# Optimization experiments

Measured on AMD Instinct MI355X. Metric: run time of the kernel, lower is better.

## Reference

```python
import jax, jax.numpy as jnp
from jax import lax
import numpy as np

N, K, F, H, NG, T = 32768, 16, 64, 128, 1024, 2


def setup_inputs() -> dict:
    key = jax.random.key(0)
    ks = jax.random.split(key, 24)
    def rn(k, shape, s=0.05):
        return jax.random.normal(k, shape, jnp.float32) * s
    inp = {
        'n': jax.random.normal(ks[0], (N, F), jnp.float32),
        'nbr': jax.random.randint(ks[1], (N, K), 0, N),
        # deterministic sorted graph ids -> every graph non-empty (safe segment_max)
        'gid': (jnp.arange(N) * NG) // N,
        'G': NG,
        # SAGEConv layer 1: LSTM(F,F), fc_self/fc_neigh F->H
        'lstm1_Wih': rn(ks[2], (F, 4 * F)), 'lstm1_Whh': rn(ks[3], (F, 4 * F)), 'lstm1_b': jnp.zeros((4 * F,), jnp.float32),
        'fcs1_W': rn(ks[4], (F, H)), 'fcs1_b': jnp.zeros((H,), jnp.float32),
        'fcn1_W': rn(ks[5], (F, H)), 'fcn1_b': jnp.zeros((H,), jnp.float32),
        # SAGEConv layer 2: LSTM(H,H), fc_self/fc_neigh H->H
        'lstm2_Wih': rn(ks[6], (H, 4 * H)), 'lstm2_Whh': rn(ks[7], (H, 4 * H)), 'lstm2_b': jnp.zeros((4 * H,), jnp.float32),
        'fcs2_W': rn(ks[8], (H, H)), 'fcs2_b': jnp.zeros((H,), jnp.float32),
        'fcn2_W': rn(ks[9], (H, H)), 'fcn2_b': jnp.zeros((H,), jnp.float32),
        # WeightedSumAndMax atom weighting: H->1
        'rw_W': rn(ks[10], (H, 1)), 'rw_b': jnp.zeros((1,), jnp.float32),
        # task head: 2H->H, H->T
        'h1_W': rn(ks[11], (2 * H, H)), 'h1_b': jnp.zeros((H,), jnp.float32),
        'h2_W': rn(ks[12], (H, T)), 'h2_b': jnp.zeros((T,), jnp.float32),
    }
    return inp


def _lstm_last(xseq, Wih, Whh, b):
    # xseq: [N, K, Fin]; returns last hidden state [N, Hh]
    Hh = Whh.shape[0]
    h0 = jnp.zeros((xseq.shape[0], Hh), xseq.dtype)
    def step(carry, xt):
        h, c = carry
        g = xt @ Wih + h @ Whh + b  # [N, 4H], torch gate order i,f,g,o
        i, f, gg, o = jnp.split(g, 4, axis=-1)
        c = jax.nn.sigmoid(f) * c + jax.nn.sigmoid(i) * jnp.tanh(gg)
        h = jax.nn.sigmoid(o) * jnp.tanh(c)
        return (h, c), None
    (h, _), _ = lax.scan(step, (h0, h0), jnp.swapaxes(xseq, 0, 1))
    return h


def _sage_layer(x, nbr, Wih, Whh, b, Ws, bs, Wn, bn):
    hn = _lstm_last(x[nbr], Wih, Whh, b)          # LSTM aggregate of neighbors
    return jax.nn.sigmoid(x @ Ws + bs + hn @ Wn + bn)


def reference(n, nbr, gid, G,
              lstm1_Wih, lstm1_Whh, lstm1_b, fcs1_W, fcs1_b, fcn1_W, fcn1_b,
              lstm2_Wih, lstm2_Whh, lstm2_b, fcs2_W, fcs2_b, fcn2_W, fcn2_b,
              rw_W, rw_b, h1_W, h1_b, h2_W, h2_b):
    G = int(G)
    h1 = _sage_layer(n, nbr, lstm1_Wih, lstm1_Whh, lstm1_b, fcs1_W, fcs1_b, fcn1_W, fcn1_b)
    h2 = _sage_layer(h1, nbr, lstm2_Wih, lstm2_Whh, lstm2_b, fcs2_W, fcs2_b, fcn2_W, fcn2_b)
    # WeightedSumAndMax readout
    w = jax.nn.sigmoid(h2 @ rw_W + rw_b)                       # [N,1]
    wsum = jax.ops.segment_sum(w * h2, gid, num_segments=G)    # [G,H]
    mx = jax.ops.segment_max(h2, gid, num_segments=G)          # [G,H]
    gemb = jnp.concatenate([wsum, mx], axis=-1)                # [G,2H]
    y = jax.nn.sigmoid(gemb @ h1_W + h1_b)
    y = jax.nn.sigmoid(y @ h2_W + h2_b)                        # classification
    return y
```

## Files before the change

### kernel.cpp

```cpp
#include <hip/hip_runtime.h>

typedef unsigned short u16;
typedef __attribute__((ext_vector_type(8))) short bf16x8;
typedef __attribute__((ext_vector_type(4))) float f32x4;
typedef __attribute__((ext_vector_type(2))) float f32x2;

constexpr int N_ = 32768;
constexpr int H_ = 128;
constexpr int G_ = 1024;
constexpr int T_ = 2;

__device__ __forceinline__ float sigf(float x){
  float e = __builtin_amdgcn_exp2f(x * -1.44269504f);
  return __builtin_amdgcn_rcpf(1.0f + e);
}
__device__ __forceinline__ f32x2 sig2(f32x2 x){
  f32x2 t = x * -1.44269504f;
  f32x2 e; e.x = __builtin_amdgcn_exp2f(t.x); e.y = __builtin_amdgcn_exp2f(t.y);
  f32x2 d = e + 1.0f;
  f32x2 r; r.x = __builtin_amdgcn_rcpf(d.x); r.y = __builtin_amdgcn_rcpf(d.y);
  return r;
}
__device__ __forceinline__ f32x2 tanh2(f32x2 x){
  f32x2 t = x * 2.88539008f;
  f32x2 e; e.x = __builtin_amdgcn_exp2f(t.x); e.y = __builtin_amdgcn_exp2f(t.y);
  f32x2 d = e + 1.0f;
  f32x2 r; r.x = __builtin_amdgcn_rcpf(d.x); r.y = __builtin_amdgcn_rcpf(d.y);
  return 1.0f - 2.0f*r;
}
__device__ __forceinline__ u16 f2bf(float f){
  unsigned u = __float_as_uint(f);
  unsigned r = (u + 0x7FFFu + ((u>>16)&1u))>>16;
  return (u16)r;
}
__device__ __forceinline__ unsigned cvt_pk_bf16(float a, float b){
  unsigned r;
  asm("v_cvt_pk_bf16_f32 %0, %1, %2" : "=v"(r) : "v"(a), "v"(b));
  return r;
}
__device__ __forceinline__ float bf2f(u16 h){ return __uint_as_float(((unsigned)h)<<16); }
__device__ __forceinline__ float asf(unsigned u){ return __uint_as_float(u); }
__device__ __forceinline__ f32x4 mfma16(bf16x8 a, bf16x8 b, f32x4 c){
  return __builtin_amdgcn_mfma_f32_16x16x32_bf16(a,b,c,0,0,0);
}

__global__ __launch_bounds__(64)
void pack_all(const float* __restrict__ l1Wih, const float* __restrict__ fcs1W,
              const float* __restrict__ l1Whh, const float* __restrict__ fcn1W,
              const float* __restrict__ l2Wih, const float* __restrict__ fcs2W,
              const float* __restrict__ l2Whh, const float* __restrict__ fcn2W,
              const float* __restrict__ l1b, const float* __restrict__ bs1,
              const float* __restrict__ bn1,
              const float* __restrict__ l2b, const float* __restrict__ bs2,
              const float* __restrict__ bn2,
              u16* BY1, u16* BW1, u16* BN1, u16* BY2, u16* BW2, u16* BN2,
              u16* bY1, u16* bY2)
{
  int b = blockIdx.x;
  const int lane = threadIdx.x;
  if (b == 416) {
    for (int i = lane; i < 1024; i += 64) {
      if (i < 384) {
        int p = i; float v;
        if (p < 256) { int o = (p&3)*64 + ((p>>6)<<4) + ((p>>2)&15); v = l1b[o]; }
        else         { int j = p-256; v = bs1[j] + bn1[j]; }
        bY1[p] = f2bf(v);
      } else {
        int p = i - 384; float v;
        if (p < 512) { int o = (p&3)*128 + ((p>>6)<<4) + ((p>>2)&15); v = l2b[o]; }
        else         { int j = p-512; v = bs2[j] + bn2[j]; }
        bY2[p] = f2bf(v);
      }
    }
    return;
  }
  const float* src; u16* dst; int srcNC, NTtot, ntOff, ntCnt, Fh, perm;
  if      (b < 32)  { src=l1Wih; dst=BY1; srcNC=256; NTtot=24; ntOff=0;  ntCnt=16; Fh=64;  perm=2; }
  else if (b < 48)  { src=fcs1W; dst=BY1; srcNC=128; NTtot=24; ntOff=16; ntCnt=8;  Fh=0;   perm=0; b-=32; }
  else if (b < 80)  { src=l1Whh; dst=BW1; srcNC=256; NTtot=16; ntOff=0;  ntCnt=16; Fh=64;  perm=1; b-=48; }
  else if (b < 96)  { src=fcn1W; dst=BN1; srcNC=128; NTtot=8;  ntOff=0;  ntCnt=8;  Fh=0;   perm=0; b-=80; }
  else if (b < 224) { src=l2Wih; dst=BY2; srcNC=512; NTtot=40; ntOff=0;  ntCnt=32; Fh=128; perm=2; b-=96; }
  else if (b < 256) { src=fcs2W; dst=BY2; srcNC=128; NTtot=40; ntOff=32; ntCnt=8;  Fh=0;   perm=0; b-=224; }
  else if (b < 384) { src=l2Whh; dst=BW2; srcNC=512; NTtot=32; ntOff=0;  ntCnt=32; Fh=128; perm=1; b-=256; }
  else              { src=fcn2W; dst=BN2; srcNC=128; NTtot=8;  ntOff=0;  ntCnt=8;  Fh=0;   perm=0; b-=384; }
  const int ntl = b % ntCnt, kt = b / ntCnt;
  const int n = lane & 15, qq = lane >> 4;
  int pr = ntl*16 + n;
  int o;
  if (perm == 1)      o = ((pr>>4)&3)*Fh + ((pr>>6)<<4) + (pr&15);
  else if (perm == 2) o = (pr&3)*Fh + ((pr>>6)<<4) + ((pr>>2)&15);
  else                o = pr;
  u16* d = dst + ((size_t)((kt*NTtot + ntOff + ntl)*64 + lane))*8;
#pragma unroll
  for (int j = 0; j < 8; ++j) {
    int k = kt*32 + qq*8 + j;
    d[j] = f2bf(src[(size_t)k*srcNC + o]);
  }
}

template<int KT, int NTT, int AF32>
__global__ __launch_bounds__(256, 2)
void gemm_kernel(const void* __restrict__ Ain,
                 const u16* __restrict__ Bpk,
                 const u16* __restrict__ biasbf,
                 u16* __restrict__ out, int out_stride)
{
  constexpr int KA  = KT*32;
  constexpr int NTW = NTT/4;
  constexpr int STR = KA + 8;
  __shared__ __align__(16) u16 a_lds[32*STR];
  const int tid  = threadIdx.x;
  const int base = blockIdx.x*32;
  {
    const int sub = tid & 7, rowl = tid >> 3;
    if constexpr (AF32) {
      const float* src = (const float*)Ain + (size_t)(base+rowl)*KA;
#pragma unroll
      for (int cc = 0; cc < KA/32; ++cc) {
        int e0 = (cc*8+sub)*4;
        float4 v = *(const float4*)(src + e0);
        ushort4 bv;
        bv.x = f2bf(v.x); bv.y = f2bf(v.y); bv.z = f2bf(v.z); bv.w = f2bf(v.w);
        *(ushort4*)(void*)(a_lds + rowl*STR + e0) = bv;
      }
    } else {
      const u16* src = (const u16*)Ain + (size_t)(base+rowl)*KA;
#pragma unroll
      for (int cc = 0; cc < KA/64; ++cc) {
        int e0 = (cc*8+sub)*8;
        uint4 v = *(const uint4*)(const void*)(src + e0);
        *(uint4*)(void*)(a_lds + rowl*STR + e0) = v;
      }
    }
  }
  __syncthreads();
  const int lane = tid & 63, w = tid >> 6;
  const int lc = lane & 15, q = lane >> 4;
  f32x4 acc[2][NTW];
  f32x4 z = {0.f,0.f,0.f,0.f};
#pragma unroll
  for (int m = 0; m < 2; ++m)
#pragma unroll
    for (int j = 0; j < NTW; ++j) acc[m][j] = z;
#pragma unroll
  for (int kt = 0; kt < KT; ++kt) {
    bf16x8 af0 = *(const bf16x8*)(const void*)(a_lds + lc*STR      + kt*32 + q*8);
    bf16x8 af1 = *(const bf16x8*)(const void*)(a_lds + (lc+16)*STR + kt*32 + q*8);
#pragma unroll
    for (int j = 0; j < NTW; ++j) {
      bf16x8 bf = *(const bf16x8*)(const void*)(Bpk + ((size_t)((kt*NTT + w*NTW + j)*64 + lane))*8);
      acc[0][j] = mfma16(af0, bf, acc[0][j]);
      acc[1][j] = mfma16(af1, bf, acc[1][j]);
    }
  }
#pragma unroll
  for (int m = 0; m < 2; ++m)
#pragma unroll
    for (int j = 0; j < NTW; ++j) {
      int col = (w*NTW + j)*16 + lc;
#pragma unroll
      for (int r = 0; r < 4; ++r) {
        int row = base + m*16 + q*4 + r;
        out[(size_t)row*out_stride + col] = f2bf(acc[m][j][r] + bf2f(biasbf[col]));
      }
    }
}

template<int KT>
__global__ __launch_bounds__(KT*128, 4)
void lstm_kernel(const int* __restrict__ nbr,
                 const u16* __restrict__ Y, int nctot,
                 const u16* __restrict__ Bpk,
                 const u16* __restrict__ BN,
                 const u16* __restrict__ Sp, int s_stride, int s_coloff,
                 u16* __restrict__ out)
{
  constexpr int F   = KT*32;
  constexpr int NW  = KT*2;
  constexpr int NTT = KT*8;
  constexpr int STR = F + 8;
  __shared__ __align__(16) u16 h_lds[2][32*STR];
  __shared__ int nbr_s[512];
  const int tid  = threadIdx.x;
  const int base = blockIdx.x*32;
  const int lane = tid & 63, w = tid >> 6;
  const int lc = lane & 15, q = lane >> 4;

  for (int i = tid; i < 512; i += NW*64) nbr_s[i] = nbr[base*16 + i];

  bf16x8 bfr[KT][4];
#pragma unroll
  for (int kt = 0; kt < KT; ++kt)
#pragma unroll
    for (int g = 0; g < 4; ++g)
      bfr[kt][g] = *(const bf16x8*)(const void*)(Bpk + ((size_t)((kt*NTT + w*4 + g)*64 + lane))*8);

  f32x2 cs[2][2];
#pragma unroll
  for (int m = 0; m < 2; ++m)
#pragma unroll
    for (int rp = 0; rp < 2; ++rp) cs[m][rp] = (f32x2){0.f, 0.f};
  __syncthreads();

  const char* Yb = (const char*)Y;
  const unsigned rowbytes = (unsigned)nctot * 2u;
  const unsigned lanebyte = (unsigned)(w*64 + lc*4) * 2u;
  const int wcol = w*16 + lc;

  uint2 yv[2][4];
#pragma unroll
  for (int m = 0; m < 2; ++m)
#pragma unroll
    for (int r = 0; r < 4; ++r) {
      unsigned vr = (unsigned)nbr_s[(m*16 + q*4 + r)*16 + 0];
      yv[m][r] = *(const uint2*)(const void*)(Yb + (vr*rowbytes + lanebyte));
    }

  for (int t = 0; t < 16; ++t) {
    const u16* hr = h_lds[t & 1];
    u16*       hw = h_lds[(t & 1) ^ 1];
#pragma unroll
    for (int m = 0; m < 2; ++m) {
      f32x4 acc[4];
      f32x4 z = {0.f,0.f,0.f,0.f};
#pragma unroll
      for (int g = 0; g < 4; ++g) acc[g] = z;
      if (t != 0) {
#pragma unroll
        for (int kt = 0; kt < KT; ++kt) {
          bf16x8 af = *(const bf16x8*)(const void*)(hr + (lc + m*16)*STR + kt*32 + q*8);
#pragma unroll
          for (int g = 0; g < 4; ++g) acc[g] = mfma16(af, bfr[kt][g], acc[g]);
        }
      }
#pragma unroll
      for (int rp = 0; rp < 2; ++rp) {
        uint2 ya = yv[m][2*rp], yb = yv[m][2*rp+1];
        f32x2 yi = { asf(ya.x<<16),          asf(yb.x<<16) };
        f32x2 yf = { asf(ya.x&0xffff0000u),  asf(yb.x&0xffff0000u) };
        f32x2 yg = { asf(ya.y<<16),          asf(yb.y<<16) };
        f32x2 yo = { asf(ya.y&0xffff0000u),  asf(yb.y&0xffff0000u) };
        f32x2 gi = (f32x2){acc[0][2*rp], acc[0][2*rp+1]} + yi;
        f32x2 gf = (f32x2){acc[1][2*rp], acc[1][2*rp+1]} + yf;
        f32x2 gg = (f32x2){acc[2][2*rp], acc[2][2*rp+1]} + yg;
        f32x2 go = (f32x2){acc[3][2*rp], acc[3][2*rp+1]} + yo;
        f32x2 c  = sig2(gf)*cs[m][rp] + sig2(gi)*tanh2(gg);
        cs[m][rp] = c;
        f32x2 hh = sig2(go)*tanh2(c);
        unsigned pkd = cvt_pk_bf16(hh.x, hh.y);
        int r0 = m*16 + q*4 + 2*rp;
        hw[r0*STR + wcol]     = (u16)pkd;
        hw[(r0+1)*STR + wcol] = (u16)(pkd >> 16);
      }
    }
    if (t < 15) {
#pragma unroll
      for (int m = 0; m < 2; ++m)
#pragma unroll
        for (int r = 0; r < 4; ++r) {
          unsigned vr = (unsigned)nbr_s[(m*16 + q*4 + r)*16 + t + 1];
          yv[m][r] = *(const uint2*)(const void*)(Yb + (vr*rowbytes + lanebyte));
        }
    }
    __syncthreads();
  }

  constexpr int CPW = 8 / NW;
  const u16* hf = h_lds[0];
#pragma unroll
  for (int cc2 = 0; cc2 < CPW; ++cc2) {
    const int nt = w*CPW + cc2;
    f32x4 a2[2];
    f32x4 z = {0.f,0.f,0.f,0.f};
    a2[0] = z; a2[1] = z;
#pragma unroll
    for (int kt = 0; kt < KT; ++kt) {
      bf16x8 nf = *(const bf16x8*)(const void*)(BN + ((size_t)((kt*8 + nt)*64 + lane))*8);
#pragma unroll
      for (int m = 0; m < 2; ++m) {
        bf16x8 af = *(const bf16x8*)(const void*)(hf + (lc + m*16)*STR + kt*32 + q*8);
        a2[m] = mfma16(af, nf, a2[m]);
      }
    }
    const int col = nt*16 + lc;
#pragma unroll
    for (int m = 0; m < 2; ++m)
#pragma unroll
      for (int r = 0; r < 4; ++r) {
        int row = base + m*16 + q*4 + r;
        float v = a2[m][r] + bf2f(Sp[(size_t)row*s_stride + s_coloff + col]);
        out[(size_t)row*H_ + col] = f2bf(sigf(v));
      }
  }
}

__global__ __launch_bounds__(128)
void head_kernel(const u16* __restrict__ h2, const float* __restrict__ rwW,
                 const float* __restrict__ rwb,
                 const float* __restrict__ h1W, const float* __restrict__ h1b,
                 const float* __restrict__ h2W, const float* __restrict__ h2b,
                 float* __restrict__ out)
{
  __shared__ float h2s[32*H_];
  __shared__ float part[32*4];
  __shared__ float wv[32];
  __shared__ float gemb[2*H_];
  __shared__ float y1[H_];
  const int g = blockIdx.x, t = threadIdx.x;
  for (int r = 0; r < 32; ++r)
    h2s[r*H_ + t] = bf2f(h2[(size_t)(g*32 + r)*H_ + t]);
  __syncthreads();
  { int r = t>>2, qq = t&3; float p = 0.f;
    for (int h = qq*32; h < qq*32+32; ++h) p += h2s[r*H_+h]*rwW[h];
    part[r*4+qq] = p; }
  __syncthreads();
  if (t < 32) wv[t] = sigf(part[t*4]+part[t*4+1]+part[t*4+2]+part[t*4+3]+rwb[0]);
  __syncthreads();
  { float wsum=0.f, mx=-3.402823466e38f;
    for (int r = 0; r < 32; ++r) { float v = h2s[r*H_+t]; wsum += wv[r]*v; mx = fmaxf(mx,v); }
    gemb[t]=wsum; gemb[H_+t]=mx; }
  __syncthreads();
  { float a = h1b[t];
    for (int k = 0; k < 2*H_; ++k) a += gemb[k]*h1W[k*H_+t];
    y1[t]=sigf(a); }
  __syncthreads();
  if (t < T_) {
    float a = h2b[t];
    for (int h = 0; h < H_; ++h) a += y1[h]*h2W[h*T_+t];
    out[(size_t)g*T_+t] = sigf(a);
  }
}

extern "C" void kernel_launch(void* const* d_in, const int* in_sizes, int n_in,
                              void* d_out, int out_size, void* d_ws, size_t ws_size,
                              hipStream_t stream) {
  const float* n_feat = (const float*)d_in[0];
  const int*   nbr    = (const int*)d_in[1];
  const float* l1Wih = (const float*)d_in[4];
  const float* l1Whh = (const float*)d_in[5];
  const float* l1b   = (const float*)d_in[6];
  const float* fcs1W = (const float*)d_in[7];
  const float* fcs1b = (const float*)d_in[8];
  const float* fcn1W = (const float*)d_in[9];
  const float* fcn1b = (const float*)d_in[10];
  const float* l2Wih = (const float*)d_in[11];
  const float* l2Whh = (const float*)d_in[12];
  const float* l2b   = (const float*)d_in[13];
  const float* fcs2W = (const float*)d_in[14];
  const float* fcs2b = (const float*)d_in[15];
  const float* fcn2W = (const float*)d_in[16];
  const float* fcn2b = (const float*)d_in[17];
  const float* rwW   = (const float*)d_in[18];
  const float* rwb   = (const float*)d_in[19];
  const float* h1W   = (const float*)d_in[20];
  const float* h1b   = (const float*)d_in[21];
  const float* h2W   = (const float*)d_in[22];
  const float* h2b   = (const float*)d_in[23];

  char* ws = (char*)d_ws;
  u16* Y   = (u16*)(ws);
  u16* h1  = (u16*)(ws + 41943040);
  u16* h2  = (u16*)(ws + 50331648);
  char* wt = ws + 58720256;
  u16* BY1 = (u16*)(wt);
  u16* BW1 = (u16*)(wt + 49152);
  u16* BN1 = (u16*)(wt + 81920);
  u16* BY2 = (u16*)(wt + 98304);
  u16* BW2 = (u16*)(wt + 262144);
  u16* BN2 = (u16*)(wt + 393216);
  u16* bY1 = (u16*)(wt + 425984);
  u16* bY2 = (u16*)(wt + 426752);

  pack_all<<<417, 64, 0, stream>>>(l1Wih, fcs1W, l1Whh, fcn1W,
                                   l2Wih, fcs2W, l2Whh, fcn2W,
                                   l1b, fcs1b, fcn1b, l2b, fcs2b, fcn2b,
                                   BY1, BW1, BN1, BY2, BW2, BN2, bY1, bY2);

  gemm_kernel<2,24,1><<<1024, 256, 0, stream>>>(n_feat, BY1, bY1, Y, 384);
  lstm_kernel<2><<<1024, 256, 0, stream>>>(nbr, Y, 384, BW1, BN1, Y, 384, 256, h1);

  gemm_kernel<4,40,0><<<1024, 256, 0, stream>>>(h1, BY2, bY2, Y, 640);
  lstm_kernel<4><<<1024, 512, 0, stream>>>(nbr, Y, 640, BW2, BN2, Y, 640, 512, h2);

  head_kernel<<<G_, 128, 0, stream>>>(h2, rwW, rwb, h1W, h1b, h2W, h2b, (float*)d_out);
}
```

Before: 311.7 us.

## Parameterize LSTM row tile and halve layer-2 tile; share reciprocal in sigmoid/tanh

Adds an MT template parameter to the LSTM kernel so the number of 16-row tiles per block is configurable. The layer-2 LSTM now processes 16 nodes per block across 2048 blocks instead of 32 nodes across 1024, which raises block count and cuts per-thread registers for more parallelism, but halves reuse of the preloaded weight fragments. Separately, the paired sigmoid and tanh helpers compute one reciprocal of the product of the two denominators instead of two reciprocals. That trades an rcp for multiplies but risks overflow or precision loss when the exponentials are large.

```diff
diff --git a/kernel.cpp b/kernel.cpp
--- a/kernel.cpp
+++ b/kernel.cpp
@@ -18,15 +18,16 @@
   f32x2 t = x * -1.44269504f;
   f32x2 e; e.x = __builtin_amdgcn_exp2f(t.x); e.y = __builtin_amdgcn_exp2f(t.y);
   f32x2 d = e + 1.0f;
-  f32x2 r; r.x = __builtin_amdgcn_rcpf(d.x); r.y = __builtin_amdgcn_rcpf(d.y);
-  return r;
+  float r = __builtin_amdgcn_rcpf(d.x * d.y);
+  return (f32x2){r * d.y, r * d.x};
 }
 __device__ __forceinline__ f32x2 tanh2(f32x2 x){
   f32x2 t = x * 2.88539008f;
   f32x2 e; e.x = __builtin_amdgcn_exp2f(t.x); e.y = __builtin_amdgcn_exp2f(t.y);
   f32x2 d = e + 1.0f;
-  f32x2 r; r.x = __builtin_amdgcn_rcpf(d.x); r.y = __builtin_amdgcn_rcpf(d.y);
-  return 1.0f - 2.0f*r;
+  float r = __builtin_amdgcn_rcpf(d.x * d.y);
+  f32x2 rr = (f32x2){r * d.y, r * d.x};
+  return 1.0f - 2.0f*rr;
 }
 __device__ __forceinline__ u16 f2bf(float f){
   unsigned u = __float_as_uint(f);
@@ -166,7 +167,7 @@
     }
 }
 
-template<int KT>
+template<int KT, int MT>
 __global__ __launch_bounds__(KT*128, 4)
 void lstm_kernel(const int* __restrict__ nbr,
                  const u16* __restrict__ Y, int nctot,
@@ -179,14 +180,15 @@
   constexpr int NW  = KT*2;
   constexpr int NTT = KT*8;
   constexpr int STR = F + 8;
-  __shared__ __align__(16) u16 h_lds[2][32*STR];
-  __shared__ int nbr_s[512];
+  constexpr int M   = MT*16;
+  __shared__ __align__(16) u16 h_lds[2][M*STR];
+  __shared__ int nbr_s[M*16];
   const int tid  = threadIdx.x;
-  const int base = blockIdx.x*32;
+  const int base = blockIdx.x * M;
   const int lane = tid & 63, w = tid >> 6;
   const int lc = lane & 15, q = lane >> 4;
 
-  for (int i = tid; i < 512; i += NW*64) nbr_s[i] = nbr[base*16 + i];
+  for (int i = tid; i < M*16; i += NW*64) nbr_s[i] = nbr[base*16 + i];
 
   bf16x8 bfr[KT][4];
 #pragma unroll
@@ -195,9 +197,9 @@
     for (int g = 0; g < 4; ++g)
       bfr[kt][g] = *(const bf16x8*)(const void*)(Bpk + ((size_t)((kt*NTT + w*4 + g)*64 + lane))*8);
 
-  f32x2 cs[2][2];
-#pragma unroll
-  for (int m = 0; m < 2; ++m)
+  f32x2 cs[MT][2];
+#pragma unroll
+  for (int m = 0; m < MT; ++m)
 #pragma unroll
     for (int rp = 0; rp < 2; ++rp) cs[m][rp] = (f32x2){0.f, 0.f};
   __syncthreads();
@@ -207,12 +209,12 @@
   const unsigned lanebyte = (unsigned)(w*64 + lc*4) * 2u;
   const int wcol = w*16 + lc;
 
-  uint2 yv[2][4];
-#pragma unroll
-  for (int m = 0; m < 2; ++m)
+  uint2 yv[MT][4];
+#pragma unroll
+  for (int m = 0; m < MT; ++m)
 #pragma unroll
     for (int r = 0; r < 4; ++r) {
-      unsigned vr = (unsigned)nbr_s[(m*16 + q*4 + r)*16 + 0];
+      unsigned vr = (unsigned)nbr_s[(m*16 + q*4 + r)*16];
       yv[m][r] = *(const uint2*)(const void*)(Yb + (vr*rowbytes + lanebyte));
     }
 
@@ -220,7 +222,7 @@
     const u16* hr = h_lds[t & 1];
     u16*       hw = h_lds[(t & 1) ^ 1];
 #pragma unroll
-    for (int m = 0; m < 2; ++m) {
+    for (int m = 0; m < MT; ++m) {
       f32x4 acc[4];
       f32x4 z = {0.f,0.f,0.f,0.f};
 #pragma unroll
@@ -255,7 +257,7 @@
     }
     if (t < 15) {
 #pragma unroll
-      for (int m = 0; m < 2; ++m)
+      for (int m = 0; m < MT; ++m)
 #pragma unroll
         for (int r = 0; r < 4; ++r) {
           unsigned vr = (unsigned)nbr_s[(m*16 + q*4 + r)*16 + t + 1];
@@ -270,21 +272,22 @@
 #pragma unroll
   for (int cc2 = 0; cc2 < CPW; ++cc2) {
     const int nt = w*CPW + cc2;
-    f32x4 a2[2];
+    f32x4 a2[MT];
     f32x4 z = {0.f,0.f,0.f,0.f};
-    a2[0] = z; a2[1] = z;
+#pragma unroll
+    for (int m = 0; m < MT; ++m) a2[m] = z;
 #pragma unroll
     for (int kt = 0; kt < KT; ++kt) {
       bf16x8 nf = *(const bf16x8*)(const void*)(BN + ((size_t)((kt*8 + nt)*64 + lane))*8);
 #pragma unroll
-      for (int m = 0; m < 2; ++m) {
+      for (int m = 0; m < MT; ++m) {
         bf16x8 af = *(const bf16x8*)(const void*)(hf + (lc + m*16)*STR + kt*32 + q*8);
         a2[m] = mfma16(af, nf, a2[m]);
       }
     }
     const int col = nt*16 + lc;
 #pragma unroll
-    for (int m = 0; m < 2; ++m)
+    for (int m = 0; m < MT; ++m)
 #pragma unroll
       for (int r = 0; r < 4; ++r) {
         int row = base + m*16 + q*4 + r;
@@ -377,10 +380,10 @@
                                    BY1, BW1, BN1, BY2, BW2, BN2, bY1, bY2);
 
   gemm_kernel<2,24,1><<<1024, 256, 0, stream>>>(n_feat, BY1, bY1, Y, 384);
-  lstm_kernel<2><<<1024, 256, 0, stream>>>(nbr, Y, 384, BW1, BN1, Y, 384, 256, h1);
+  lstm_kernel<2,2><<<1024, 256, 0, stream>>>(nbr, Y, 384, BW1, BN1, Y, 384, 256, h1);
 
   gemm_kernel<4,40,0><<<1024, 256, 0, stream>>>(h1, BY2, bY2, Y, 640);
-  lstm_kernel<4><<<1024, 512, 0, stream>>>(nbr, Y, 640, BW2, BN2, Y, 640, 512, h2);
+  lstm_kernel<4,1><<<2048, 512, 0, stream>>>(nbr, Y, 640, BW2, BN2, Y, 640, 512, h2);
 
   head_kernel<<<G_, 128, 0, stream>>>(h2, rwW, rwb, h1W, h1b, h2W, h2b, (float*)d_out);
 }
```

Measured after the change: 304.7 us. 2.2% less time.
